# Kernel tuning notes

Hardware: AMD Instinct MI355X
Metric: run time of the kernel (lower is better)

## Reference

```python
import jax, jax.numpy as jnp
import numpy as np

B = 4096          # batch_size
D = 256           # embedding dim
N = 2 * B
TEMPERATURE = 0.5
GAMMA = 2.0
ALPHA = 0.25


def _negative_indices():
    # Static column indices of negatives per row: all columns except self (i)
    # and the positive partner ((i+B) mod N). Shape (N, N-2).
    idx = []
    for i in range(N):
        partner = (i + B) % N
        cols = [j for j in range(N) if j != i and j != partner]
        idx.append(cols)
    return np.asarray(idx, dtype=np.int32)

_NEG_IDX = jnp.asarray(_negative_indices())


def setup_inputs() -> dict:
    key = jax.random.key(0)
    kx, ky = jax.random.split(key)
    zx = jax.random.normal(kx, (B, D), dtype=jnp.float32)
    zy = jax.random.normal(ky, (B, D), dtype=jnp.float32)
    return {"zx": zx, "zy": zy}


def reference(zx, zy):
    z = jnp.concatenate([zx, zy], axis=0)                    # (N, D)
    zn = z / jnp.linalg.norm(z, axis=1, keepdims=True)       # cosine normalize
    sim = (zn @ zn.T) / TEMPERATURE                          # (N, N)

    sim_xy = jnp.diagonal(sim, offset=B)                     # (B,)
    sim_yx = jnp.diagonal(sim, offset=-B)                    # (B,)
    pos = jnp.concatenate([sim_xy, sim_yx])[:, None]         # (N, 1)
    neg = jnp.take_along_axis(sim, _NEG_IDX, axis=1)         # (N, N-2)

    logits = jnp.concatenate([pos, neg], axis=1)             # (N, N-1)
    # CE with label 0 for every row: -log_softmax(logits)[:, 0]
    ce = jax.nn.logsumexp(logits, axis=1) - logits[:, 0]
    pt = jnp.exp(-ce)
    focal = (1.0 - pt) ** GAMMA * ce
    return (ALPHA * focal).mean()
```

## Files before the change

kernel.cpp:

```cpp
#include <hip/hip_runtime.h>
#include <stdint.h>
#include <stddef.h>


typedef __attribute__((ext_vector_type(8))) short short8;
typedef __attribute__((ext_vector_type(4))) float f32x4;

#define NROWS 8192
#define DDIM 256
#define NTILES 2080
#define NBLK 512

__device__ __forceinline__ unsigned short f2bf(float f) {
  unsigned int u = __float_as_uint(f);
  u = (u + 0x7FFFu + ((u >> 16) & 1u)) >> 16;
  return (unsigned short)u;
}

__device__ __forceinline__ void unrank_tile(int t, int& p_out, int& q_out) {
  int p = (int)((129.0f - sqrtf((float)(16641 - 8 * t))) * 0.5f);
  p = max(0, min(63, p));
  while ((((p + 1) * (129 - (p + 1))) >> 1) <= t) ++p;
  while (((p * (129 - p)) >> 1) > t) --p;
  p_out = p;
  q_out = p + (t - ((p * (129 - p)) >> 1));
}

__global__ __launch_bounds__(256) void norm_kernel(const float* __restrict__ zx,
                                                   const float* __restrict__ zy,
                                                   unsigned short* __restrict__ zn,
                                                   unsigned int* __restrict__ counter) {
  if (blockIdx.x == 0 && threadIdx.x == 0) *counter = 0u;
  const int row = blockIdx.x * 4 + (threadIdx.x >> 6);
  const int lane = threadIdx.x & 63;
  const float* src = (row < 4096) ? (zx + (size_t)row * DDIM)
                                  : (zy + (size_t)(row - 4096) * DDIM);
  float4 v = reinterpret_cast<const float4*>(src)[lane];
  float ss = v.x * v.x + v.y * v.y + v.z * v.z + v.w * v.w;
#pragma unroll
  for (int m = 1; m < 64; m <<= 1) ss += __shfl_xor(ss, m);
  const float sc = 1.69864360f * rsqrtf(ss);
  ushort4 o;
  o.x = f2bf(v.x * sc); o.y = f2bf(v.y * sc);
  o.z = f2bf(v.z * sc); o.w = f2bf(v.w * sc);
  reinterpret_cast<ushort4*>(zn + (size_t)row * DDIM)[lane] = o;
}

__global__ __launch_bounds__(256, 2) void simtri_kernel(const unsigned short* __restrict__ zn,
                                                        float* __restrict__ partial,
                                                        float* __restrict__ pos) {
  __shared__ unsigned short smem[2][2][128 * 64];
  const int c = (blockIdx.x & 7) * 64 + (blockIdx.x >> 3);
  int start, nt;
  if (c < 32) { start = c * 5;              nt = 5; }
  else        { start = 160 + (c - 32) * 4; nt = 4; }

  const int tid = threadIdx.x;
  const int lane = tid & 63;
  const int wid = tid >> 6;
  const int wr = wid >> 1;
  const int wc = wid & 1;
  const int hi = lane >> 4, lo = lane & 15;
  const int sw = lo & 7;

  const f32x4 z4 = {0.f, 0.f, 0.f, 0.f};
  f32x4 acc[4][4];
#pragma unroll
  for (int m = 0; m < 4; ++m)
#pragma unroll
    for (int n = 0; n < 4; ++n) acc[m][n] = z4;

  auto stage_one = [&](int buf, int which, int row0, int k0) {
    unsigned short* lb = &smem[buf][which][0];
#pragma unroll
    for (int j = 0; j < 4; ++j) {
      const int u = j * 256 + tid;
      const int r = u >> 3, ul = u & 7;
      const unsigned short* g =
          zn + (size_t)(row0 + r) * DDIM + k0 + ((ul ^ (r & 7)) << 3);
      unsigned short* l = lb + (size_t)(j * 256 + wid * 64) * 8;
      __builtin_amdgcn_global_load_lds(
          (const __attribute__((address_space(1))) void*)g,
          (__attribute__((address_space(3))) void*)l, 16, 0, 0);
    }
  };
  auto stageT = [&](int buf, int p, int q, int k0) {
    stage_one(buf, 0, p << 7, k0);
    if (p != q) stage_one(buf, 1, q << 7, k0);
  };

  int cp, cq;
  unrank_tile(start, cp, cq);
  stageT(0, cp, cq, 0);
  __syncthreads();

  int buf = 0;
  for (int i = 0; i < nt; ++i) {
    int np = cp, nq = cq;
    const bool have_next = (i + 1 < nt);
    if (have_next) { if (cq == 63) { np = cp + 1; nq = np; } else { nq = cq + 1; } }
    const bool isdiag = (cp == cq);
    const bool ispos = (cq == cp + 32);
    const int R0 = cp << 7;
    const int C0 = cq << 7;

#pragma unroll
    for (int kk = 0; kk < 4; ++kk) {
      if (kk < 3) stageT(buf ^ 1, cp, cq, (kk + 1) * 64);
      else if (have_next) stageT(buf ^ 1, np, nq, 0);
      const unsigned short* A = &smem[buf][0][0];
      const unsigned short* Bm = isdiag ? A : &smem[buf][1][0];
#pragma unroll
      for (int ks = 0; ks < 2; ++ks) {
        short8 af[4], bfr[4];
#pragma unroll
        for (int m = 0; m < 4; ++m)
          af[m] = *reinterpret_cast<const short8*>(
              A + ((wr * 64 + m * 16 + lo) * 64 + (((ks * 4 + hi) ^ sw) << 3)));
#pragma unroll
        for (int n = 0; n < 4; ++n)
          bfr[n] = *reinterpret_cast<const short8*>(
              Bm + ((wc * 64 + n * 16 + lo) * 64 + (((ks * 4 + hi) ^ sw) << 3)));
#pragma unroll
        for (int m = 0; m < 4; ++m)
#pragma unroll
          for (int n = 0; n < 4; ++n)
            acc[m][n] = __builtin_amdgcn_mfma_f32_16x16x32_bf16(af[m], bfr[n], acc[m][n], 0, 0, 0);
      }
      buf ^= 1;
      if (kk < 3) __syncthreads();
    }

    float rsum[4][4];
    float csum[4];
#pragma unroll
    for (int m = 0; m < 4; ++m)
#pragma unroll
      for (int r = 0; r < 4; ++r) rsum[m][r] = 0.f;
#pragma unroll
    for (int n = 0; n < 4; ++n) csum[n] = 0.f;

#pragma unroll
    for (int m = 0; m < 4; ++m)
#pragma unroll
      for (int n = 0; n < 4; ++n)
#pragma unroll
        for (int r = 0; r < 4; ++r) {
          const float e = __builtin_amdgcn_exp2f(acc[m][n][r]);
          rsum[m][r] += e;
          csum[n] += e;
        }

    if ((isdiag || ispos) && (wr == wc)) {
#pragma unroll
      for (int m = 0; m < 4; ++m)
#pragma unroll
        for (int r = 0; r < 4; ++r)
          if (lo == 4 * hi + r) {
            if (isdiag) rsum[m][r] -= __builtin_amdgcn_exp2f(acc[m][m][r]);
            else        pos[R0 + wr * 64 + m * 16 + lo] = acc[m][m][r];
          }
    }

#pragma unroll
    for (int m = 0; m < 4; ++m)
#pragma unroll
      for (int r = 0; r < 4; ++r) {
        float s = rsum[m][r];
        s += __shfl_xor(s, 1); s += __shfl_xor(s, 2);
        s += __shfl_xor(s, 4); s += __shfl_xor(s, 8);
        if (lo == 0) {
          const int grow = R0 + wr * 64 + m * 16 + (hi << 2) + r;
          partial[(size_t)(cq * 2 + wc) * NROWS + grow] = s;
        }
      }

    if (!isdiag) {
#pragma unroll
      for (int n = 0; n < 4; ++n) {
        float cs = csum[n];
        cs += __shfl_xor(cs, 16); cs += __shfl_xor(cs, 32);
        if (lane < 16)
          partial[(size_t)(cp * 2 + wr) * NROWS + (C0 + wc * 64 + n * 16 + lane)] = cs;
      }
    }

#pragma unroll
    for (int m = 0; m < 4; ++m)
#pragma unroll
      for (int n = 0; n < 4; ++n) acc[m][n] = z4;

    __syncthreads();
    cp = np; cq = nq;
  }
}

__global__ __launch_bounds__(256) void d1_kernel(const float* __restrict__ partial,
                                                 const float* __restrict__ pos,
                                                 float* __restrict__ bsum,
                                                 float* __restrict__ out,
                                                 unsigned int* __restrict__ counter) {
  const int row = blockIdx.x * 256 + threadIdx.x;
  float s = 0.f;
#pragma unroll 16
  for (int c = 0; c < 128; ++c) s += partial[(size_t)c * NROWS + row];
  const float L = __log2f(s) - pos[row & 4095];
  const float pt = __builtin_amdgcn_exp2f(-L);
  const float ce = 0.69314718056f * L;
  float f = (1.f - pt) * (1.f - pt) * ce;
#pragma unroll
  for (int m = 1; m < 64; m <<= 1) f += __shfl_xor(f, m);
  __shared__ float wsum[4];
  if ((threadIdx.x & 63) == 0) wsum[threadIdx.x >> 6] = f;
  __syncthreads();
  if (threadIdx.x == 0) {
    bsum[blockIdx.x] = wsum[0] + wsum[1] + wsum[2] + wsum[3];
    __threadfence();
    if (atomicAdd(counter, 1u) == 31u) {
      __threadfence();
      float v = 0.f;
#pragma unroll
      for (int c = 0; c < 32; ++c) v += ((const volatile float*)bsum)[c];
      out[0] = 0.25f * v / 8192.f;
    }
  }
}

extern "C" void kernel_launch(void* const* d_in, const int* in_sizes, int n_in,
                              void* d_out, int out_size, void* d_ws, size_t ws_size,
                              hipStream_t stream) {
  const float* zx = (const float*)d_in[0];
  const float* zy = (const float*)d_in[1];
  float* out = (float*)d_out;

  unsigned short* zn = (unsigned short*)d_ws;
  float* pos = (float*)((char*)d_ws + (size_t)NROWS * DDIM * 2);
  float* partial = pos + 4096;
  float* bsum = partial + (size_t)128 * NROWS;
  unsigned int* counter = (unsigned int*)(bsum + 32);

  norm_kernel<<<2048, 256, 0, stream>>>(zx, zy, zn, counter);
  simtri_kernel<<<NBLK, 256, 0, stream>>>(zn, partial, pos);
  d1_kernel<<<32, 256, 0, stream>>>(partial, pos, bsum, out, counter);
}
```

Baseline: 104.9 us.

## Reorder tile schedule for balanced pairing and stash partial sums in LDS

Replaces the row-major upper-triangle tile enumeration with a folded column-pair ordering, where each column j is paired with its mirror 63-j. This allows a closed-form start-tile decode instead of the sqrt-based unrank. Per-tile row and column partial sums now go into an LDS stash and are written to global memory after the block's tile loop finishes, instead of with scattered stores after each tile. The aim is to keep global writes out of the MFMA loop and balance the per-block schedule, at the cost of 10KB more shared memory, which could lower occupancy.

```diff
diff --git a/kernel.cpp b/kernel.cpp
--- a/kernel.cpp
+++ b/kernel.cpp
@@ -8,22 +8,12 @@
 
 #define NROWS 8192
 #define DDIM 256
-#define NTILES 2080
 #define NBLK 512
 
 __device__ __forceinline__ unsigned short f2bf(float f) {
   unsigned int u = __float_as_uint(f);
   u = (u + 0x7FFFu + ((u >> 16) & 1u)) >> 16;
   return (unsigned short)u;
-}
-
-__device__ __forceinline__ void unrank_tile(int t, int& p_out, int& q_out) {
-  int p = (int)((129.0f - sqrtf((float)(16641 - 8 * t))) * 0.5f);
-  p = max(0, min(63, p));
-  while ((((p + 1) * (129 - (p + 1))) >> 1) <= t) ++p;
-  while (((p * (129 - p)) >> 1) > t) --p;
-  p_out = p;
-  q_out = p + (t - ((p * (129 - p)) >> 1));
 }
 
 __global__ __launch_bounds__(256) void norm_kernel(const float* __restrict__ zx,
@@ -50,10 +40,23 @@
                                                         float* __restrict__ partial,
                                                         float* __restrict__ pos) {
   __shared__ unsigned short smem[2][2][128 * 64];
+  __shared__ float stash[5][4][128];
   const int c = (blockIdx.x & 7) * 64 + (blockIdx.x >> 3);
-  int start, nt;
-  if (c < 32) { start = c * 5;              nt = 5; }
-  else        { start = 160 + (c - 32) * 4; nt = 4; }
+  const int cl = c & 63;
+  const int nt = ((cl & 15) == 0) ? 5 : 4;
+  const int start = 4 * c + 4 * (c >> 6) + ((cl + 15) >> 4);
+
+  int cp, cq;
+  {
+    const int j = start / 65, r = start - j * 65;
+    if (r <= j) { cp = r; cq = j; } else { cp = r - j - 1; cq = 63 - j; }
+  }
+  const int p0 = cp, q0 = cq;
+  auto advance = [&](int& p, int& q) {
+    if (p < q) { ++p; return; }
+    p = 0;
+    q = (q < 32) ? (63 - q) : (64 - q);
+  };
 
   const int tid = threadIdx.x;
   const int lane = tid & 63;
@@ -89,8 +92,6 @@
     if (p != q) stage_one(buf, 1, q << 7, k0);
   };
 
-  int cp, cq;
-  unrank_tile(start, cp, cq);
   stageT(0, cp, cq, 0);
   __syncthreads();
 
@@ -98,11 +99,10 @@
   for (int i = 0; i < nt; ++i) {
     int np = cp, nq = cq;
     const bool have_next = (i + 1 < nt);
-    if (have_next) { if (cq == 63) { np = cp + 1; nq = np; } else { nq = cq + 1; } }
+    if (have_next) advance(np, nq);
     const bool isdiag = (cp == cq);
     const bool ispos = (cq == cp + 32);
     const int R0 = cp << 7;
-    const int C0 = cq << 7;
 
 #pragma unroll
     for (int kk = 0; kk < 4; ++kk) {
@@ -139,7 +139,6 @@
       for (int r = 0; r < 4; ++r) rsum[m][r] = 0.f;
 #pragma unroll
     for (int n = 0; n < 4; ++n) csum[n] = 0.f;
-
 #pragma unroll
     for (int m = 0; m < 4; ++m)
 #pragma unroll
@@ -150,7 +149,6 @@
           rsum[m][r] += e;
           csum[n] += e;
         }
-
     if ((isdiag || ispos) && (wr == wc)) {
 #pragma unroll
       for (int m = 0; m < 4; ++m)
@@ -161,7 +159,6 @@
             else        pos[R0 + wr * 64 + m * 16 + lo] = acc[m][m][r];
           }
     }
-
 #pragma unroll
     for (int m = 0; m < 4; ++m)
 #pragma unroll
@@ -169,19 +166,14 @@
         float s = rsum[m][r];
         s += __shfl_xor(s, 1); s += __shfl_xor(s, 2);
         s += __shfl_xor(s, 4); s += __shfl_xor(s, 8);
-        if (lo == 0) {
-          const int grow = R0 + wr * 64 + m * 16 + (hi << 2) + r;
-          partial[(size_t)(cq * 2 + wc) * NROWS + grow] = s;
-        }
+        if (lo == 0) stash[i][wc][wr * 64 + m * 16 + (hi << 2) + r] = s;
       }
-
     if (!isdiag) {
 #pragma unroll
       for (int n = 0; n < 4; ++n) {
         float cs = csum[n];
         cs += __shfl_xor(cs, 16); cs += __shfl_xor(cs, 32);
-        if (lane < 16)
-          partial[(size_t)(cp * 2 + wr) * NROWS + (C0 + wc * 64 + n * 16 + lane)] = cs;
+        if (lane < 16) stash[i][2 + wr][wc * 64 + n * 16 + lane] = cs;
       }
     }
 
@@ -192,6 +184,19 @@
 
     __syncthreads();
     cp = np; cq = nq;
+  }
+
+  __syncthreads();
+  {
+    int fp = p0, fq = q0;
+    const int half = tid >> 7;
+    const int rr = tid & 127;
+    for (int i = 0; i < nt; ++i) {
+      partial[(size_t)(fq * 2 + half) * NROWS + fp * 128 + rr] = stash[i][half][rr];
+      if (fp != fq)
+        partial[(size_t)(fp * 2 + half) * NROWS + fq * 128 + rr] = stash[i][2 + half][rr];
+      advance(fp, fq);
+    }
   }
 }
 
```

Result: slower. 108.7 us (+3.7%).
